# Kernel tuning notes

Measured on AMD Instinct MI355X. Metric: run time of the kernel, lower is better.

## Reference

```python
import jax, jax.numpy as jnp
from jax import lax
import numpy as np

INPUT_SIZE, HIDDEN, NUM_LAYERS = 64, 512, 2
BATCH, SEQ = 256, 512


def setup_inputs() -> dict:
    key = jax.random.key(0)
    ks = jax.random.split(key, 16)
    k_lim = 1.0 / np.sqrt(HIDDEN)  # torch LSTMCell init range
    u = lambda k, shape: jax.random.uniform(k, shape, jnp.float32, -k_lim, k_lim)
    inp = {"x": jax.random.normal(ks[0], (BATCH, SEQ, INPUT_SIZE), jnp.float32)}
    for layer in range(NUM_LAYERS):
        in_size = INPUT_SIZE if layer == 0 else HIDDEN
        base = 1 + 4 * layer
        inp[f"W_ih{layer}"] = u(ks[base + 0], (4 * HIDDEN, in_size))
        inp[f"W_hh{layer}"] = u(ks[base + 1], (4 * HIDDEN, HIDDEN))
        inp[f"b_ih{layer}"] = u(ks[base + 2], (4 * HIDDEN,))
        inp[f"b_hh{layer}"] = u(ks[base + 3], (4 * HIDDEN,))
    inp["fc_w"] = u(ks[10], (1, HIDDEN))
    inp["fc_b"] = u(ks[11], (1,))
    return inp


def _lstm_layer(xs, W_ih, W_hh, b_ih, b_hh):
    """xs: [T, B, in] -> (hs [T, B, H], h_last [B, H])."""
    H = W_hh.shape[1]
    B = xs.shape[1]
    # Input projection for all timesteps at once (one big GEMM).
    pre = jnp.einsum('tbi,gi->tbg', xs, W_ih) + b_ih + b_hh  # [T, B, 4H]

    def step(carry, p):
        h, c = carry
        gates = p + h @ W_hh.T  # [B, 4H], gate order i,f,g,o
        i, f, g, o = jnp.split(gates, 4, axis=-1)
        i, f, o = jax.nn.sigmoid(i), jax.nn.sigmoid(f), jax.nn.sigmoid(o)
        c = f * c + i * jnp.tanh(g)
        h = o * jnp.tanh(c)
        return (h, c), h

    init = (jnp.zeros((B, H), xs.dtype), jnp.zeros((B, H), xs.dtype))
    (h_last, _), hs = lax.scan(step, init, pre)
    return hs, h_last


def reference(x, W_ih0, W_hh0, b_ih0, b_hh0, W_ih1, W_hh1, b_ih1, b_hh1, fc_w, fc_b):
    params = [(W_ih0, W_hh0, b_ih0, b_hh0), (W_ih1, W_hh1, b_ih1, b_hh1)]
    xs = jnp.transpose(x, (1, 0, 2))  # [T, B, in]
    h_last = None
    for (W_ih, W_hh, b_ih, b_hh) in params:
        xs, h_last = _lstm_layer(xs, W_ih, W_hh, b_ih, b_hh)
    # dropout p=0.0 / eval mode -> identity
    return (h_last @ fc_w.T + fc_b)[:, 0]  # [B]
```

## Files before the change

kernel.cpp:

```cpp
#include <hip/hip_runtime.h>
#include <math.h>

#define T_SEQ 512
#define BATCH 256
#define HID   512
#define IN0   64
#define K1    1024
#define K0    576
#define NWG   256
#define NTHR  256
#define LDS_DYN 131072

typedef _Float16 f16x8 __attribute__((ext_vector_type(8)));
typedef float    f32x4 __attribute__((ext_vector_type(4)));

__device__ __forceinline__ float sigm(float x)   { return 1.0f / (1.0f + __expf(-x)); }
__device__ __forceinline__ float tanh_f(float x) { return 2.0f / (1.0f + __expf(-2.0f * x)) - 1.0f; }

__device__ __forceinline__ f32x4 mfma16(f16x8 a, f16x8 b, f32x4 c) {
  return __builtin_amdgcn_mfma_f32_16x16x32_f16(a, b, c, 0, 0, 0);
}

__device__ __forceinline__ void store_short_wt(const _Float16* p, unsigned v) {
  asm volatile("global_store_short %0, %1, off sc0 sc1"
               :: "v"((const void*)p), "v"(v) : "memory");
}
__device__ __forceinline__ void store_dword_wt(const unsigned* p, unsigned v) {
  asm volatile("global_store_dword %0, %1, off sc0 sc1"
               :: "v"((const void*)p), "v"(v) : "memory");
}

__global__ void k_split_w(const float* __restrict__ Wih, const float* __restrict__ Whh,
                          const float* __restrict__ bih, const float* __restrict__ bhh,
                          _Float16* __restrict__ whi, float* __restrict__ bias, int Kin) {
  int K = Kin + HID;
  long idx = (long)blockIdx.x * 256 + threadIdx.x;
  long total = 2048L * K;
  if (idx < total) {
    int k = (int)(idx % K);
    int r = (int)(idx / K);
    int gate = r & 3, hcol = r >> 2;
    int row = gate * HID + hcol;
    float v = (k < Kin) ? Wih[(long)row * Kin + k] : Whh[(long)row * HID + (k - Kin)];
    long o = (long)(r >> 4) * 16 * K + (long)(k >> 3) * 128 + (r & 15) * 8 + (k & 7);
    whi[o] = (_Float16)v;
  }
  if (idx < 2048) {
    int r = (int)idx;
    int gate = r & 3, hcol = r >> 2;
    int row = gate * HID + hcol;
    bias[r] = bih[row] + bhh[row];
  }
}

__global__ void k_split_x(const float* __restrict__ x, _Float16* __restrict__ x16) {
  int idx = blockIdx.x * 256 + threadIdx.x;
  int i = idx & 63;
  int b = (idx >> 6) & 255;
  int t = idx >> 14;
  x16[idx] = (_Float16)x[((size_t)b * T_SEQ + t) * IN0 + i];
}

__device__ __forceinline__ void grid_barrier(unsigned* bar, unsigned epoch) {
  __syncthreads();
  if (threadIdx.x == 0) {
    const unsigned g = blockIdx.x & 7;
    unsigned a = __hip_atomic_fetch_add(&bar[32 + g * 32], 1u,
                                        __ATOMIC_RELAXED, __HIP_MEMORY_SCOPE_AGENT);
    if (a == epoch * 32u - 1u) {
      unsigned t = __hip_atomic_fetch_add(&bar[0], 1u,
                                          __ATOMIC_RELAXED, __HIP_MEMORY_SCOPE_AGENT);
      if (t == epoch * 8u - 1u) {
        #pragma unroll
        for (int gg = 0; gg < 8; ++gg)
          store_dword_wt(&bar[512 + gg * 32], epoch);
      }
    }
    while ((int)(__hip_atomic_load(&bar[512 + g * 32],
                                   __ATOMIC_RELAXED, __HIP_MEMORY_SCOPE_AGENT) - epoch) < 0)
      __builtin_amdgcn_s_sleep(4);
    __builtin_amdgcn_fence(__ATOMIC_ACQUIRE, "agent");
  }
  __syncthreads();
}

__global__ __launch_bounds__(NTHR, 1) void k_lstm(
    const _Float16* __restrict__ x16,
    const _Float16* __restrict__ w0, const float* __restrict__ bias0,
    const _Float16* __restrict__ w1, const float* __restrict__ bias1,
    _Float16* __restrict__ in1,
    const float* __restrict__ fcw, const float* __restrict__ fcb,
    float* __restrict__ out, unsigned* __restrict__ bar)
{
  extern __shared__ __align__(16) _Float16 ldsA[];

  const int tid  = threadIdx.x;
  const int lane = tid & 63;
  const int wv   = __builtin_amdgcn_readfirstlane(tid >> 6);
  const int wg   = blockIdx.x;
  const int layer1 = (wg < 128) ? 1 : 0;
  const int lw   = wg & 127;
  const int rg   = lw >> 2;
  const int bg   = lw & 3;
  const int bbase = bg * 64 + wv * 16;
  const int lr = lane & 15;
  const int lg = lane >> 4;
  const int KW = layer1 ? K1 : K0;

  {
    const f16x8* gw = reinterpret_cast<const f16x8*>((layer1 ? w1 : w0) + (size_t)rg * 64 * KW);
    f16x8* lw16 = reinterpret_cast<f16x8*>(ldsA);
    const int nch = 8 * KW;
    for (int ch = tid; ch < nch; ch += NTHR) lw16[ch] = gw[ch];
  }
  __syncthreads();

  const float* bsrc = layer1 ? bias1 : bias0;
  float4 b4[4];
  int hcv[4];
  #pragma unroll
  for (int sl = 0; sl < 4; ++sl) {
    hcv[sl] = rg * 16 + sl * 4 + lg;
    b4[sl] = *reinterpret_cast<const float4*>(bsrc + hcv[sl] * 4);
  }
  const f16x8* A = reinterpret_cast<const f16x8*>(ldsA);

  float c[4] = {0.f, 0.f, 0.f, 0.f};

  #pragma unroll 1
  for (int n = 0; n <= T_SEQ; ++n) {
    const int pr = (n + 1) & 1;
    const int pw = n & 1;
    const bool active = layer1 ? (n >= 1) : (n < T_SEQ);
    if (active) {
      f32x4 acc[4];
      #pragma unroll
      for (int sl = 0; sl < 4; ++sl) {
        acc[sl][0]=b4[sl].x; acc[sl][1]=b4[sl].y; acc[sl][2]=b4[sl].z; acc[sl][3]=b4[sl].w;
      }

      const _Float16* Bp = in1 + ((size_t)pr * BATCH + bbase) * K1 + (size_t)lr * K1 + lg * 8;

      if (layer1) {
        f16x8 bufA[16], bufB[16];
        #pragma unroll
        for (int kk = 0; kk < 16; ++kk)
          bufA[kk] = *reinterpret_cast<const f16x8*>(Bp + (size_t)kk * 32);
        #pragma unroll
        for (int kk = 0; kk < 16; ++kk)
          bufB[kk] = *reinterpret_cast<const f16x8*>(Bp + (size_t)(16 + kk) * 32);
        #pragma unroll
        for (int kk = 0; kk < 16; ++kk) {
          const int ac = (kk * 4 + lg) * 16 + lr;
          #pragma unroll
          for (int sl = 0; sl < 4; ++sl)
            acc[sl] = mfma16(A[(size_t)sl * 2 * K1 + ac], bufA[kk], acc[sl]);
        }
        #pragma unroll
        for (int kk = 0; kk < 16; ++kk) {
          const int ac = ((16 + kk) * 4 + lg) * 16 + lr;
          #pragma unroll
          for (int sl = 0; sl < 4; ++sl)
            acc[sl] = mfma16(A[(size_t)sl * 2 * K1 + ac], bufB[kk], acc[sl]);
        }
      } else {
        const _Float16* Xp = x16 + ((size_t)n * BATCH + bbase) * IN0 + (size_t)lr * IN0 + lg * 8;
        f16x8 xb[2];
        xb[0] = *reinterpret_cast<const f16x8*>(Xp);
        xb[1] = *reinterpret_cast<const f16x8*>(Xp + 32);
        f16x8 bufA[16];
        #pragma unroll
        for (int kk = 0; kk < 16; ++kk)
          bufA[kk] = *reinterpret_cast<const f16x8*>(Bp + (size_t)kk * 32);
        #pragma unroll
        for (int ks = 0; ks < 2; ++ks) {
          const int ac = (ks * 4 + lg) * 16 + lr;
          #pragma unroll
          for (int sl = 0; sl < 4; ++sl)
            acc[sl] = mfma16(A[(size_t)sl * 2 * K0 + ac], xb[ks], acc[sl]);
        }
        #pragma unroll
        for (int kk = 0; kk < 16; ++kk) {
          const int ac = (8 + kk * 4 + lg) * 16 + lr;
          #pragma unroll
          for (int sl = 0; sl < 4; ++sl)
            acc[sl] = mfma16(A[(size_t)sl * 2 * K0 + ac], bufA[kk], acc[sl]);
        }
      }

      const int b = bbase + lr;
      #pragma unroll
      for (int sl = 0; sl < 4; ++sl) {
        float i_ = sigm(acc[sl][0]);
        float f_ = sigm(acc[sl][1]);
        float g_ = tanh_f(acc[sl][2]);
        float o_ = sigm(acc[sl][3]);
        c[sl] = fmaf(f_, c[sl], i_ * g_);
        float hv = o_ * tanh_f(c[sl]);
        _Float16 h16 = (_Float16)hv;
        const int col = (layer1 ? 512 : 0) + hcv[sl];
        const size_t idx = ((size_t)pw * BATCH + b) * K1 + col;
        store_short_wt(in1 + idx, (unsigned)__builtin_bit_cast(unsigned short, h16));
      }
      asm volatile("s_waitcnt vmcnt(0)" ::: "memory");
    }
    grid_barrier(bar, (unsigned)(n + 1));
  }

  if (wg == 0 && tid < BATCH) {
    const _Float16* r = in1 + (size_t)tid * K1 + 512;
    float acc = 0.f;
    #pragma unroll 8
    for (int k = 0; k < HID; ++k)
      acc = fmaf((float)r[k], fcw[k], acc);
    out[tid] = acc + fcb[0];
  }
}

extern "C" void kernel_launch(void* const* d_in, const int* in_sizes, int n_in,
                              void* d_out, int out_size, void* d_ws, size_t ws_size,
                              hipStream_t stream) {
  const float* x    = (const float*)d_in[0];
  const float* Wih0 = (const float*)d_in[1];
  const float* Whh0 = (const float*)d_in[2];
  const float* bih0 = (const float*)d_in[3];
  const float* bhh0 = (const float*)d_in[4];
  const float* Wih1 = (const float*)d_in[5];
  const float* Whh1 = (const float*)d_in[6];
  const float* bih1 = (const float*)d_in[7];
  const float* bhh1 = (const float*)d_in[8];
  const float* fcw  = (const float*)d_in[9];
  const float* fcb  = (const float*)d_in[10];

  char* ws = (char*)d_ws;
  size_t off = 0;
  auto alloc = [&](size_t bytes) -> char* {
    char* pp = ws + off;
    off = (off + bytes + 1023) & ~(size_t)1023;
    return pp;
  };
  unsigned*  bar  = (unsigned*)alloc(4096);
  _Float16* x16  = (_Float16*)alloc((size_t)T_SEQ * BATCH * IN0 * 2);
  _Float16* w0   = (_Float16*)alloc((size_t)2048 * K0 * 2);
  _Float16* w1   = (_Float16*)alloc((size_t)2048 * K1 * 2);
  float*    bias0 = (float*)alloc(2048 * 4);
  float*    bias1 = (float*)alloc(2048 * 4);
  _Float16* in1  = (_Float16*)alloc((size_t)2 * BATCH * K1 * 2);

  (void)hipFuncSetAttribute(reinterpret_cast<const void*>(k_lstm),
                            hipFuncAttributeMaxDynamicSharedMemorySize, LDS_DYN);

  (void)hipMemsetAsync(bar, 0, 4096, stream);
  (void)hipMemsetAsync(in1, 0, (size_t)2 * BATCH * K1 * 2, stream);
  k_split_x<<<(T_SEQ * BATCH * IN0) / 256, 256, 0, stream>>>(x, x16);
  k_split_w<<<(int)((2048L * K0 + 255) / 256), 256, 0, stream>>>(Wih0, Whh0, bih0, bhh0, w0, bias0, IN0);
  k_split_w<<<(int)((2048L * K1 + 255) / 256), 256, 0, stream>>>(Wih1, Whh1, bih1, bhh1, w1, bias1, HID);
  k_lstm<<<NWG, NTHR, LDS_DYN, stream>>>(x16, w0, bias0, w1, bias1,
                                         in1, fcw, fcb, (float*)d_out, bar);
}
```

Baseline: 4.817 ms.

## Split grid barrier into four independent batch-group domains

Replaces the global two-level grid barrier with four independent flat barriers, one per batch group (wg & 3). Work-groups that share a batch slice only need each other's hidden states, so each group synchronises only with its 64 peers. The spin-wait sleep is shortened, and a final wait on all domains is added before the FC reduction. Scheduling barriers are also inserted so the operand loads are issued before the MFMA chains. The risk is more contention on each 64-way atomic counter and a correctness dependence on the batch-to-domain mapping.

```diff
diff --git a/kernel.cpp b/kernel.cpp
--- a/kernel.cpp
+++ b/kernel.cpp
@@ -61,24 +61,16 @@
   x16[idx] = (_Float16)x[((size_t)b * T_SEQ + t) * IN0 + i];
 }
 
-__device__ __forceinline__ void grid_barrier(unsigned* bar, unsigned epoch) {
+__device__ __forceinline__ void grid_barrier(unsigned* bar, unsigned epoch, unsigned dom) {
   __syncthreads();
   if (threadIdx.x == 0) {
-    const unsigned g = blockIdx.x & 7;
-    unsigned a = __hip_atomic_fetch_add(&bar[32 + g * 32], 1u,
+    unsigned a = __hip_atomic_fetch_add(&bar[dom * 32], 1u,
                                         __ATOMIC_RELAXED, __HIP_MEMORY_SCOPE_AGENT);
-    if (a == epoch * 32u - 1u) {
-      unsigned t = __hip_atomic_fetch_add(&bar[0], 1u,
-                                          __ATOMIC_RELAXED, __HIP_MEMORY_SCOPE_AGENT);
-      if (t == epoch * 8u - 1u) {
-        #pragma unroll
-        for (int gg = 0; gg < 8; ++gg)
-          store_dword_wt(&bar[512 + gg * 32], epoch);
-      }
-    }
-    while ((int)(__hip_atomic_load(&bar[512 + g * 32],
+    if (a == epoch * 64u - 1u)
+      store_dword_wt(&bar[256 + dom * 32], epoch);
+    while ((int)(__hip_atomic_load(&bar[256 + dom * 32],
                                    __ATOMIC_RELAXED, __HIP_MEMORY_SCOPE_AGENT) - epoch) < 0)
-      __builtin_amdgcn_s_sleep(4);
+      __builtin_amdgcn_s_sleep(1);
     __builtin_amdgcn_fence(__ATOMIC_ACQUIRE, "agent");
   }
   __syncthreads();
@@ -102,6 +94,7 @@
   const int lw   = wg & 127;
   const int rg   = lw >> 2;
   const int bg   = lw & 3;
+  const unsigned dom = (unsigned)(wg & 3);
   const int bbase = bg * 64 + wv * 16;
   const int lr = lane & 15;
   const int lg = lane >> 4;
@@ -149,6 +142,7 @@
         #pragma unroll
         for (int kk = 0; kk < 16; ++kk)
           bufB[kk] = *reinterpret_cast<const f16x8*>(Bp + (size_t)(16 + kk) * 32);
+        __builtin_amdgcn_sched_barrier(0);
         #pragma unroll
         for (int kk = 0; kk < 16; ++kk) {
           const int ac = (kk * 4 + lg) * 16 + lr;
@@ -172,6 +166,7 @@
         #pragma unroll
         for (int kk = 0; kk < 16; ++kk)
           bufA[kk] = *reinterpret_cast<const f16x8*>(Bp + (size_t)kk * 32);
+        __builtin_amdgcn_sched_barrier(0);
         #pragma unroll
         for (int ks = 0; ks < 2; ++ks) {
           const int ac = (ks * 4 + lg) * 16 + lr;
@@ -204,16 +199,28 @@
       }
       asm volatile("s_waitcnt vmcnt(0)" ::: "memory");
     }
-    grid_barrier(bar, (unsigned)(n + 1));
-  }
-
-  if (wg == 0 && tid < BATCH) {
-    const _Float16* r = in1 + (size_t)tid * K1 + 512;
-    float acc = 0.f;
-    #pragma unroll 8
-    for (int k = 0; k < HID; ++k)
-      acc = fmaf((float)r[k], fcw[k], acc);
-    out[tid] = acc + fcb[0];
+    grid_barrier(bar, (unsigned)(n + 1), dom);
+  }
+
+  if (wg == 0) {
+    if (tid == 0) {
+      #pragma unroll
+      for (int d = 0; d < 4; ++d)
+        while ((int)(__hip_atomic_load(&bar[256 + d * 32],
+                                       __ATOMIC_RELAXED, __HIP_MEMORY_SCOPE_AGENT)
+                     - (unsigned)(T_SEQ + 1)) < 0)
+          __builtin_amdgcn_s_sleep(1);
+      __builtin_amdgcn_fence(__ATOMIC_ACQUIRE, "agent");
+    }
+    __syncthreads();
+    if (tid < BATCH) {
+      const _Float16* r = in1 + (size_t)tid * K1 + 512;
+      float acc = 0.f;
+      #pragma unroll 8
+      for (int k = 0; k < HID; ++k)
+        acc = fmaf((float)r[k], fcw[k], acc);
+      out[tid] = acc + fcb[0];
+    }
   }
 }
 
```

Result: slower. 5.222 ms (+8.4%).
